# Performance work log

Hardware: AMD Instinct MI355X
Metric: run time of the kernel (lower is better)

Reference implementation:

```python
import jax, jax.numpy as jnp
import numpy as np

L, B, T, C = 4, 4, 2048, 1024
FFN = 4 * C
STD = 0.02
EPS = 1e-5
NEG_INF = -1e38


def setup_inputs() -> dict:
    key = jax.random.key(0)
    ks = jax.random.split(key, 18)
    n = lambda k, shape, s=STD: jax.random.normal(k, shape, jnp.float32) * s
    u = lambda k, shape: jax.random.uniform(k, shape, jnp.float32)
    return {
        "x": jax.random.normal(ks[0], (B, T, C), jnp.float32),
        "ln1_w": jnp.ones((L, C), jnp.float32),
        "tm_mix_k": u(ks[1], (L, 1, 1, C)),
        "tm_mix_v": u(ks[2], (L, 1, 1, C)),
        "tm_mix_r": u(ks[3], (L, 1, 1, C)),
        "tm_k_w": n(ks[4], (L, C, C)),
        "tm_v_w": n(ks[5], (L, C, C)),
        "tm_r_w": n(ks[6], (L, C, C)),
        "tm_o_w": n(ks[7], (L, C, C)),
        # time_decay in [-5, 1] like RWKV decay_speed init; w = -exp(time_decay)
        "time_decay": u(ks[8], (L, C)) * 6.0 - 5.0,
        "time_first": jnp.log(0.3).astype(jnp.float32) + 0.5 * jax.random.normal(ks[9], (L, C), jnp.float32),
        "ln2_w": jnp.ones((L, C), jnp.float32),
        "cm_mix_k": u(ks[10], (L, 1, 1, C)),
        "cm_mix_r": u(ks[11], (L, 1, 1, C)),
        "cm_k_w": n(ks[12], (L, FFN, C)),
        "cm_v_w": n(ks[13], (L, C, FFN)),
        "cm_r_w": n(ks[14], (L, C, C)),
        "lnf_w": jnp.ones((C,), jnp.float32),
    }


def layer_norm(x, w):
    mu = jnp.mean(x, axis=-1, keepdims=True)
    var = jnp.mean(jnp.square(x - mu), axis=-1, keepdims=True)
    return (x - mu) * jax.lax.rsqrt(var + EPS) * w


def time_shift(x):
    # ZeroPad2d((0,0,1,-1)): shift sequence right by one, zero at t=0
    return jnp.pad(x, ((0, 0), (1, 0), (0, 0)))[:, :-1]


def wkv_scan(k, v, time_decay, time_first):
    # k, v: [B, T, C]; numerically-stabilized linear WKV recurrence over T
    w = -jnp.exp(time_decay)  # [C]
    u = time_first            # [C]
    zeros = jnp.zeros(k.shape[::2], k.dtype)  # [B, C]

    def step(carry, kv):
        num, den, mx = carry
        kt, vt = kv
        max_out = jnp.maximum(mx, kt + u)
        e1 = jnp.exp(mx - max_out)
        e2 = jnp.exp(kt + u - max_out)
        out = (e1 * num + e2 * vt) / (e1 * den + e2)
        max_st = jnp.maximum(mx + w, kt)
        e1 = jnp.exp(mx + w - max_st)
        e2 = jnp.exp(kt - max_st)
        return (e1 * num + e2 * vt, e1 * den + e2, max_st), out

    init = (zeros, zeros, jnp.full_like(zeros, NEG_INF))
    _, out = jax.lax.scan(step, init, (k.swapaxes(0, 1), v.swapaxes(0, 1)))
    return out.swapaxes(0, 1)  # [B, T, C]


def reference(x, ln1_w, tm_mix_k, tm_mix_v, tm_mix_r, tm_k_w, tm_v_w, tm_r_w, tm_o_w,
              time_decay, time_first, ln2_w, cm_mix_k, cm_mix_r, cm_k_w, cm_v_w, cm_r_w, lnf_w):
    n_layer = ln1_w.shape[0]
    for l in range(n_layer):
        # --- TimeMixing ---
        h = layer_norm(x, ln1_w[l])
        prev = time_shift(h)
        k = jnp.einsum('btc,oc->bto', h * tm_mix_k[l] + prev * (1 - tm_mix_k[l]), tm_k_w[l])
        v = jnp.einsum('btc,oc->bto', h * tm_mix_v[l] + prev * (1 - tm_mix_v[l]), tm_v_w[l])
        r = jax.nn.sigmoid(jnp.einsum('btc,oc->bto', h * tm_mix_r[l] + prev * (1 - tm_mix_r[l]), tm_r_w[l]))
        wkv = wkv_scan(k, v, time_decay[l], time_first[l])
        x = x + jnp.einsum('btc,oc->bto', r * wkv, tm_o_w[l])
        # --- ChannelMixing ---
        h = layer_norm(x, ln2_w[l])
        prev = time_shift(h)
        kk = jnp.einsum('btc,fc->btf', h * cm_mix_k[l] + prev * (1 - cm_mix_k[l]), cm_k_w[l])  # [B,T,4C]
        vv = jnp.einsum('btf,of->bto', jnp.square(jax.nn.relu(kk)), cm_v_w[l])
        rr = jax.nn.sigmoid(jnp.einsum('btc,oc->bto', h * cm_mix_r[l] + prev * (1 - cm_mix_r[l]), cm_r_w[l]))
        x = x + rr * vv
    return layer_norm(x, lnf_w)
```

## Files before the change

### kernel.cpp

```cpp
#include <hip/hip_runtime.h>
#include <hip/hip_bf16.h>


#define LNUM 4
#define BSZ  4
#define TSZ  2048
#define CSZ  1024
#define FFND 4096
#define MROWS (BSZ*TSZ)
#define EPSF 1e-5f

typedef __hip_bfloat16 bf16;
typedef __bf16 bf16x8 __attribute__((ext_vector_type(8)));
typedef float f32x4 __attribute__((ext_vector_type(4)));

#define BM 128
#define BK 64

#define SCK  64
#define SLEN (TSZ/SCK)

__device__ __forceinline__ void async_copy16(const void* g, void* l) {
    __builtin_amdgcn_global_load_lds((const __attribute__((address_space(1))) void*)g,
                                     (__attribute__((address_space(3))) void*)l, 16, 0, 0);
}

template<int MODE, int TBN>
__launch_bounds__(256)
__global__ void gemm_bt(const bf16* __restrict__ A, const bf16* __restrict__ Bw,
                        void* __restrict__ outp, const bf16* __restrict__ aux,
                        int K, int N)
{
    constexpr int MT  = (TBN == 128) ? 4 : 2;
    constexpr int NBI = TBN / 32;
    __shared__ __align__(16) __bf16 sA[BM*BK];
    __shared__ __align__(16) __bf16 sB[TBN*BK];
    const int tid  = threadIdx.x;
    const int lane = tid & 63;
    const int wid  = tid >> 6;
    const int wmB  = (TBN == 128) ? (wid >> 1) * 64 : wid * 32;
    const int wnB  = (TBN == 128) ? (wid & 1) * 64 : 0;
    const size_t bm0 = (size_t)blockIdx.x * BM;
    const size_t bn0 = (size_t)blockIdx.y * TBN;

    const int lrow8 = lane >> 3;
    const int cbg   = (lane & 7) ^ lrow8;

    const bf16* pA[4]; const bf16* pB[NBI];
#pragma unroll
    for (int i = 0; i < 4; ++i)
        pA[i] = A + (bm0 + (i*4 + wid)*8 + lrow8) * (size_t)K + cbg*8;
#pragma unroll
    for (int i = 0; i < NBI; ++i)
        pB[i] = Bw + (bn0 + (i*4 + wid)*8 + lrow8) * (size_t)K + cbg*8;

    f32x4 acc[MT][4];
#pragma unroll
    for (int a = 0; a < MT; ++a)
#pragma unroll
        for (int b = 0; b < 4; ++b) acc[a][b] = (f32x4){0.f,0.f,0.f,0.f};

    const int q   = lane >> 4;
    const int rlo = lane & 15;

    const int ktiles = K / BK;
    for (int kt = 0; kt < ktiles; ++kt) {
#pragma unroll
        for (int i = 0; i < 4; ++i) {
            async_copy16(pA[i], &sA[(i*4 + wid)*8*BK]);
            pA[i] += BK;
        }
#pragma unroll
        for (int i = 0; i < NBI; ++i) {
            async_copy16(pB[i], &sB[(i*4 + wid)*8*BK]);
            pB[i] += BK;
        }
        __syncthreads();
#pragma unroll
        for (int ks = 0; ks < 2; ++ks) {
            bf16x8 aF[MT], bF[4];
#pragma unroll
            for (int mt = 0; mt < MT; ++mt) {
                const int r  = wmB + mt*16 + rlo;
                const int cb = (ks*4 + q) ^ (r & 7);
                aF[mt] = *(const bf16x8*)&sA[r*BK + cb*8];
            }
#pragma unroll
            for (int nt = 0; nt < 4; ++nt) {
                const int r  = wnB + nt*16 + rlo;
                const int cb = (ks*4 + q) ^ (r & 7);
                bF[nt] = *(const bf16x8*)&sB[r*BK + cb*8];
            }
#pragma unroll
            for (int mt = 0; mt < MT; ++mt)
#pragma unroll
                for (int nt = 0; nt < 4; ++nt)
                    acc[mt][nt] = __builtin_amdgcn_mfma_f32_16x16x32_bf16(
                        aF[mt], bF[nt], acc[mt][nt], 0, 0, 0);
        }
        __syncthreads();
    }

#pragma unroll
    for (int mt = 0; mt < MT; ++mt) {
#pragma unroll
        for (int nt = 0; nt < 4; ++nt) {
            const size_t col = bn0 + wnB + nt*16 + rlo;
#pragma unroll
            for (int i = 0; i < 4; ++i) {
                const size_t row = bm0 + wmB + mt*16 + q*4 + i;
                const size_t idx = row * (size_t)N + col;
                const float v = acc[mt][nt][i];
                if (MODE == 2) {
                    ((float*)outp)[idx] += v;
                } else if (MODE == 3) {
                    const float t = fmaxf(v, 0.f);
                    ((bf16*)outp)[idx] = __float2bfloat16(t*t);
                } else if (MODE == 4) {
                    ((bf16*)outp)[idx] = __float2bfloat16(1.f/(1.f+__expf(-v)));
                } else {
                    ((float*)outp)[idx] += (float)aux[idx] * v;
                }
            }
        }
    }
}

__launch_bounds__(256)
__global__ void gemm_kvr(const bf16* __restrict__ A0, const bf16* __restrict__ A1,
                         const bf16* __restrict__ A2,
                         const bf16* __restrict__ W0, const bf16* __restrict__ W1,
                         const bf16* __restrict__ W2,
                         bf16* __restrict__ O0, bf16* __restrict__ O1,
                         bf16* __restrict__ O2)
{
    constexpr int TBN = 64, MT = 2, NBI = 2, K = CSZ, N = CSZ;
    const int z = blockIdx.z;
    const bf16* A  = (z == 0) ? A0 : (z == 1) ? A1 : A2;
    const bf16* Bw = (z == 0) ? W0 : (z == 1) ? W1 : W2;
    bf16* outp     = (z == 0) ? O0 : (z == 1) ? O1 : O2;

    __shared__ __align__(16) __bf16 sA[BM*BK];
    __shared__ __align__(16) __bf16 sB[TBN*BK];
    const int tid  = threadIdx.x;
    const int lane = tid & 63;
    const int wid  = tid >> 6;
    const int wmB  = wid * 32;
    const size_t bm0 = (size_t)blockIdx.x * BM;
    const size_t bn0 = (size_t)blockIdx.y * TBN;

    const int lrow8 = lane >> 3;
    const int cbg   = (lane & 7) ^ lrow8;

    const bf16* pA[4]; const bf16* pB[NBI];
#pragma unroll
    for (int i = 0; i < 4; ++i)
        pA[i] = A + (bm0 + (i*4 + wid)*8 + lrow8) * (size_t)K + cbg*8;
#pragma unroll
    for (int i = 0; i < NBI; ++i)
        pB[i] = Bw + (bn0 + (i*4 + wid)*8 + lrow8) * (size_t)K + cbg*8;

    f32x4 acc[MT][4];
#pragma unroll
    for (int a = 0; a < MT; ++a)
#pragma unroll
        for (int b = 0; b < 4; ++b) acc[a][b] = (f32x4){0.f,0.f,0.f,0.f};

    const int q   = lane >> 4;
    const int rlo = lane & 15;

    for (int kt = 0; kt < K/BK; ++kt) {
#pragma unroll
        for (int i = 0; i < 4; ++i) {
            async_copy16(pA[i], &sA[(i*4 + wid)*8*BK]);
            pA[i] += BK;
        }
#pragma unroll
        for (int i = 0; i < NBI; ++i) {
            async_copy16(pB[i], &sB[(i*4 + wid)*8*BK]);
            pB[i] += BK;
        }
        __syncthreads();
#pragma unroll
        for (int ks = 0; ks < 2; ++ks) {
            bf16x8 aF[MT], bF[4];
#pragma unroll
            for (int mt = 0; mt < MT; ++mt) {
                const int r  = wmB + mt*16 + rlo;
                const int cb = (ks*4 + q) ^ (r & 7);
                aF[mt] = *(const bf16x8*)&sA[r*BK + cb*8];
            }
#pragma unroll
            for (int nt = 0; nt < 4; ++nt) {
                const int r  = nt*16 + rlo;
                const int cb = (ks*4 + q) ^ (r & 7);
                bF[nt] = *(const bf16x8*)&sB[r*BK + cb*8];
            }
#pragma unroll
            for (int mt = 0; mt < MT; ++mt)
#pragma unroll
                for (int nt = 0; nt < 4; ++nt)
                    acc[mt][nt] = __builtin_amdgcn_mfma_f32_16x16x32_bf16(
                        aF[mt], bF[nt], acc[mt][nt], 0, 0, 0);
        }
        __syncthreads();
    }

#pragma unroll
    for (int mt = 0; mt < MT; ++mt) {
#pragma unroll
        for (int nt = 0; nt < 4; ++nt) {
            const size_t col = bn0 + nt*16 + rlo;
#pragma unroll
            for (int i = 0; i < 4; ++i) {
                const size_t row = bm0 + wmB + mt*16 + q*4 + i;
                float v = acc[mt][nt][i];
                if (z == 2) v = 1.f/(1.f+__expf(-v));
                ((bf16*)outp)[row * (size_t)N + col] = __float2bfloat16(v);
            }
        }
    }
}

template<int NOUT>
__launch_bounds__(256)
__global__ void ln_mix_kernel(const float* __restrict__ x, const float* __restrict__ lnw,
                              const float* __restrict__ mka, const float* __restrict__ mva,
                              const float* __restrict__ mra,
                              bf16* __restrict__ ok, bf16* __restrict__ ov, bf16* __restrict__ orr)
{
    const int bt  = blockIdx.x;
    const int t   = bt % TSZ;
    const int tid = threadIdx.x;
    const float4 xc = ((const float4*)(x + (size_t)bt*CSZ))[tid];
    float4 xp = {0.f,0.f,0.f,0.f};
    const bool hasp = (t != 0);
    if (hasp) xp = ((const float4*)(x + (size_t)(bt-1)*CSZ))[tid];

    float s0 = xc.x+xc.y+xc.z+xc.w;
    float s1 = xc.x*xc.x+xc.y*xc.y+xc.z*xc.z+xc.w*xc.w;
    float s2 = xp.x+xp.y+xp.z+xp.w;
    float s3 = xp.x*xp.x+xp.y*xp.y+xp.z*xp.z+xp.w*xp.w;
#pragma unroll
    for (int off = 32; off > 0; off >>= 1) {
        s0 += __shfl_down(s0, off); s1 += __shfl_down(s1, off);
        s2 += __shfl_down(s2, off); s3 += __shfl_down(s3, off);
    }
    __shared__ float red[4][4];
    if ((tid & 63) == 0) { const int wq = tid >> 6;
        red[wq][0]=s0; red[wq][1]=s1; red[wq][2]=s2; red[wq][3]=s3; }
    __syncthreads();
    s0 = red[0][0]+red[1][0]+red[2][0]+red[3][0];
    s1 = red[0][1]+red[1][1]+red[2][1]+red[3][1];
    s2 = red[0][2]+red[1][2]+red[2][2]+red[3][2];
    s3 = red[0][3]+red[1][3]+red[2][3]+red[3][3];

    const float inv = 1.f/CSZ;
    const float muC = s0*inv;
    const float rsC = rsqrtf(s1*inv - muC*muC + EPSF);
    const float muP = s2*inv;
    const float rsP = rsqrtf(s3*inv - muP*muP + EPSF);

    const int c4 = tid*4;
    const float4 lw = ((const float4*)lnw)[tid];
    const float4 mk = ((const float4*)mka)[tid];
    const float4 mv = (NOUT >= 2) ? ((const float4*)mva)[tid] : lw;
    const float4 mr = (NOUT >= 3) ? ((const float4*)mra)[tid] : lw;

    float hcv[4] = {(xc.x-muC)*rsC*lw.x, (xc.y-muC)*rsC*lw.y,
                    (xc.z-muC)*rsC*lw.z, (xc.w-muC)*rsC*lw.w};
    float hpv[4];
    if (hasp) {
        hpv[0]=(xp.x-muP)*rsP*lw.x; hpv[1]=(xp.y-muP)*rsP*lw.y;
        hpv[2]=(xp.z-muP)*rsP*lw.z; hpv[3]=(xp.w-muP)*rsP*lw.w;
    } else { hpv[0]=hpv[1]=hpv[2]=hpv[3]=0.f; }
    const float mkv[4]={mk.x,mk.y,mk.z,mk.w};
    const float mvv[4]={mv.x,mv.y,mv.z,mv.w};
    const float mrv[4]={mr.x,mr.y,mr.z,mr.w};

    __align__(8) bf16 o0[4], o1[4], o2[4];
#pragma unroll
    for (int j = 0; j < 4; ++j) {
        o0[j] = __float2bfloat16(hcv[j]*mkv[j] + hpv[j]*(1.f-mkv[j]));
        if (NOUT >= 2) o1[j] = __float2bfloat16(hcv[j]*mvv[j] + hpv[j]*(1.f-mvv[j]));
        if (NOUT >= 3) o2[j] = __float2bfloat16(hcv[j]*mrv[j] + hpv[j]*(1.f-mrv[j]));
    }
    *(uint2*)(ok + (size_t)bt*CSZ + c4) = *(const uint2*)o0;
    if (NOUT >= 2) *(uint2*)(ov  + (size_t)bt*CSZ + c4) = *(const uint2*)o1;
    if (NOUT >= 3) *(uint2*)(orr + (size_t)bt*CSZ + c4) = *(const uint2*)o2;
}

__launch_bounds__(256)
__global__ void wkv_sum_kernel(const bf16* __restrict__ kb, const bf16* __restrict__ vb,
                               const float* __restrict__ td,
                               float* __restrict__ sN, float* __restrict__ sD,
                               float* __restrict__ sM)
{
    const int j  = blockIdx.x;
    const int b  = blockIdx.y >> 2;
    const int cg = blockIdx.y & 3;
    const int c  = cg*256 + threadIdx.x;
    const float w = -__expf(td[c]);

    size_t idx = ((size_t)b*TSZ + j*SLEN)*CSZ + c;
    float num = 0.f, den = 0.f, mx = -1e38f;
    float kt = (float)kb[idx], vt = (float)vb[idx];
    for (int t = 0; t < SLEN; ++t) {
        float kn = 0.f, vn = 0.f;
        if (t + 1 < SLEN) {
            kn = (float)kb[idx + CSZ]; vn = (float)vb[idx + CSZ];
        }
        const float ms = fmaxf(mx + w, kt);
        const float p1 = __expf(mx + w - ms);
        const float p2 = __expf(kt - ms);
        num = p1*num + p2*vt; den = p1*den + p2; mx = ms;
        idx += CSZ; kt = kn; vt = vn;
    }
    const size_t sidx = ((size_t)b*SCK + j)*CSZ + c;
    sN[sidx] = num; sD[sidx] = den; sM[sidx] = mx;
}

__launch_bounds__(256)
__global__ void wkv_comb_kernel(const float* __restrict__ td,
                                float* __restrict__ sN, float* __restrict__ sD,
                                float* __restrict__ sM)
{
    const int id = blockIdx.x*256 + threadIdx.x;
    const int b  = id >> 10;
    const int c  = id & (CSZ-1);
    const float wL = -__expf(td[c]) * (float)SLEN;
    float n = 0.f, d = 0.f, m = -1e38f;
    size_t idx = (size_t)b*SCK*CSZ + c;
    float nl = sN[idx], dl = sD[idx], ml = sM[idx];
    for (int j = 0; j < SCK; ++j) {
        float nn = 0.f, dn = 0.f, mn = 0.f;
        if (j + 1 < SCK) {
            nn = sN[idx + CSZ]; dn = sD[idx + CSZ]; mn = sM[idx + CSZ];
        }
        sN[idx] = n; sD[idx] = d; sM[idx] = m;
        const float mi = m + wL;
        const float mo = fmaxf(mi, ml);
        const float e1 = __expf(mi - mo);
        const float e2 = __expf(ml - mo);
        n = e1*n + e2*nl; d = e1*d + e2*dl; m = mo;
        idx += CSZ; nl = nn; dl = dn; ml = mn;
    }
}

__launch_bounds__(256)
__global__ void wkv_out_kernel(const bf16* __restrict__ kb, const bf16* __restrict__ vb,
                               const bf16* __restrict__ rb,
                               const float* __restrict__ td, const float* __restrict__ tf,
                               const float* __restrict__ sN, const float* __restrict__ sD,
                               const float* __restrict__ sM,
                               bf16* __restrict__ outb)
{
    const int j  = blockIdx.x;
    const int b  = blockIdx.y >> 2;
    const int cg = blockIdx.y & 3;
    const int c  = cg*256 + threadIdx.x;
    const float w = -__expf(td[c]);
    const float u = tf[c];

    const size_t sidx = ((size_t)b*SCK + j)*CSZ + c;
    float num = sN[sidx], den = sD[sidx], mx = sM[sidx];

    size_t idx = ((size_t)b*TSZ + j*SLEN)*CSZ + c;
    float kt = (float)kb[idx], vt = (float)vb[idx], rt = (float)rb[idx];
    for (int t = 0; t < SLEN; ++t) {
        float kn = 0.f, vn = 0.f, rn = 0.f;
        if (t + 1 < SLEN) {
            kn = (float)kb[idx + CSZ]; vn = (float)vb[idx + CSZ]; rn = (float)rb[idx + CSZ];
        }
        const float ku = kt + u;
        const float mo = fmaxf(mx, ku);
        const float e1 = __expf(mx - mo);
        const float e2 = __expf(ku - mo);
        const float outv = (e1*num + e2*vt) / (e1*den + e2);
        const float ms = fmaxf(mx + w, kt);
        const float p1 = __expf(mx + w - ms);
        const float p2 = __expf(kt - ms);
        num = p1*num + p2*vt; den = p1*den + p2; mx = ms;
        outb[idx] = __float2bfloat16(rt * outv);
        idx += CSZ; kt = kn; vt = vn; rt = rn;
    }
}

__launch_bounds__(256)
__global__ void final_ln_kernel(const float* __restrict__ x, const float* __restrict__ lnw,
                                float* __restrict__ out)
{
    const int bt  = blockIdx.x;
    const int tid = threadIdx.x;
    const float4 xc = ((const float4*)(x + (size_t)bt*CSZ))[tid];
    float s0 = xc.x+xc.y+xc.z+xc.w;
    float s1 = xc.x*xc.x+xc.y*xc.y+xc.z*xc.z+xc.w*xc.w;
#pragma unroll
    for (int off = 32; off > 0; off >>= 1) {
        s0 += __shfl_down(s0, off); s1 += __shfl_down(s1, off);
    }
    __shared__ float red[4][2];
    if ((tid & 63) == 0) { red[tid>>6][0] = s0; red[tid>>6][1] = s1; }
    __syncthreads();
    s0 = red[0][0]+red[1][0]+red[2][0]+red[3][0];
    s1 = red[0][1]+red[1][1]+red[2][1]+red[3][1];
    const float inv = 1.f/CSZ;
    const float mu = s0*inv;
    const float rs = rsqrtf(s1*inv - mu*mu + EPSF);
    const float4 lw = ((const float4*)lnw)[tid];
    float4 o;
    o.x = (xc.x-mu)*rs*lw.x; o.y = (xc.y-mu)*rs*lw.y;
    o.z = (xc.z-mu)*rs*lw.z; o.w = (xc.w-mu)*rs*lw.w;
    ((float4*)(out + (size_t)bt*CSZ))[tid] = o;
}

#define N4_CC (CSZ*CSZ/4)
#define N4_FC (FFND*CSZ/4)
__global__ void cvt_weights_kernel(const float* __restrict__ tk, const float* __restrict__ tv,
                                   const float* __restrict__ tr, const float* __restrict__ to,
                                   const float* __restrict__ ck, const float* __restrict__ cv,
                                   const float* __restrict__ cr,
                                   bf16* __restrict__ wk, bf16* __restrict__ wv,
                                   bf16* __restrict__ wr, bf16* __restrict__ wo,
                                   bf16* __restrict__ wck, bf16* __restrict__ wcv,
                                   bf16* __restrict__ wcr)
{
    int i = blockIdx.x * 256 + threadIdx.x;
    const float* s; bf16* d;
    if      (i < 1*N4_CC)          { s = tk; d = wk;  }
    else if (i < 2*N4_CC)          { s = tv; d = wv;  i -= 1*N4_CC; }
    else if (i < 3*N4_CC)          { s = tr; d = wr;  i -= 2*N4_CC; }
    else if (i < 4*N4_CC)          { s = to; d = wo;  i -= 3*N4_CC; }
    else if (i < 4*N4_CC+N4_FC)    { s = ck; d = wck; i -= 4*N4_CC; }
    else if (i < 4*N4_CC+2*N4_FC)  { s = cv; d = wcv; i -= 4*N4_CC+N4_FC; }
    else                           { s = cr; d = wcr; i -= 4*N4_CC+2*N4_FC; }
    const float4 f = ((const float4*)s)[i];
    __align__(8) bf16 o[4] = {__float2bfloat16(f.x), __float2bfloat16(f.y),
                              __float2bfloat16(f.z), __float2bfloat16(f.w)};
    ((uint2*)d)[i] = *(const uint2*)o;
}
#define CVT_TOTAL4 (4*N4_CC + 2*N4_FC + N4_CC)

static constexpr size_t SZ_XF32 = (size_t)MROWS*CSZ*4;
static constexpr size_t SZ_ABF  = (size_t)MROWS*CSZ*2;
static constexpr size_t OFF_X   = 0;
static constexpr size_t OFF_XK  = OFF_X  + SZ_XF32;
static constexpr size_t OFF_XV  = OFF_XK + SZ_ABF;
static constexpr size_t OFF_XR  = OFF_XV + SZ_ABF;
static constexpr size_t OFF_K   = OFF_XR + SZ_ABF;
static constexpr size_t OFF_V   = OFF_K  + SZ_ABF;
static constexpr size_t OFF_R   = OFF_V  + SZ_ABF;
static constexpr size_t OFF_KK  = OFF_R  + SZ_ABF;
static constexpr size_t OFF_W   = OFF_KK + (size_t)MROWS*FFND*2;
static constexpr size_t OFF_WK  = OFF_W;
static constexpr size_t OFF_WV  = OFF_WK + (size_t)CSZ*CSZ*2;
static constexpr size_t OFF_WR  = OFF_WV + (size_t)CSZ*CSZ*2;
static constexpr size_t OFF_WO  = OFF_WR + (size_t)CSZ*CSZ*2;
static constexpr size_t OFF_WCK = OFF_WO + (size_t)CSZ*CSZ*2;
static constexpr size_t OFF_WCV = OFF_WCK + (size_t)FFND*CSZ*2;
static constexpr size_t OFF_WCR = OFF_WCV + (size_t)CSZ*FFND*2;

static constexpr size_t SZ_SUM  = (size_t)BSZ*SCK*CSZ*4;

extern "C" void kernel_launch(void* const* d_in, const int* in_sizes, int n_in,
                              void* d_out, int out_size, void* d_ws, size_t ws_size,
                              hipStream_t stream)
{
    const float* xin   = (const float*)d_in[0];
    const float* ln1w  = (const float*)d_in[1];
    const float* tmixk = (const float*)d_in[2];
    const float* tmixv = (const float*)d_in[3];
    const float* tmixr = (const float*)d_in[4];
    const float* tkw   = (const float*)d_in[5];
    const float* tvw   = (const float*)d_in[6];
    const float* trw   = (const float*)d_in[7];
    const float* tow   = (const float*)d_in[8];
    const float* tdec  = (const float*)d_in[9];
    const float* tfst  = (const float*)d_in[10];
    const float* ln2w  = (const float*)d_in[11];
    const float* cmixk = (const float*)d_in[12];
    const float* cmixr = (const float*)d_in[13];
    const float* ckw   = (const float*)d_in[14];
    const float* cvw   = (const float*)d_in[15];
    const float* crw   = (const float*)d_in[16];
    const float* lnfw  = (const float*)d_in[17];

    char* ws = (char*)d_ws;
    float* xres = (float*)(ws + OFF_X);
    bf16* xk  = (bf16*)(ws + OFF_XK);
    bf16* xv  = (bf16*)(ws + OFF_XV);
    bf16* xr  = (bf16*)(ws + OFF_XR);
    bf16* kb  = (bf16*)(ws + OFF_K);
    bf16* vb  = (bf16*)(ws + OFF_V);
    bf16* rb  = (bf16*)(ws + OFF_R);
    bf16* kkb = (bf16*)(ws + OFF_KK);
    bf16* rwkv = xk;
    bf16* rr  = (bf16*)(ws + OFF_K);
    float* sN  = (float*)(ws + OFF_KK);
    float* sD  = (float*)(ws + OFF_KK + SZ_SUM);
    float* sM  = (float*)(ws + OFF_KK + 2*SZ_SUM);
    bf16* wk  = (bf16*)(ws + OFF_WK);
    bf16* wv  = (bf16*)(ws + OFF_WV);
    bf16* wr  = (bf16*)(ws + OFF_WR);
    bf16* wo  = (bf16*)(ws + OFF_WO);
    bf16* wck = (bf16*)(ws + OFF_WCK);
    bf16* wcv = (bf16*)(ws + OFF_WCV);
    bf16* wcr = (bf16*)(ws + OFF_WCR);

    hipMemcpyAsync(xres, xin, SZ_XF32, hipMemcpyDeviceToDevice, stream);

    const dim3 blk(256);
    const dim3 gKVR(MROWS/BM, CSZ/64, 3);
    const dim3 gC64(MROWS/BM, CSZ/64);
    const dim3 gF(MROWS/BM, FFND/128);
    const dim3 gScan(SCK, BSZ*4);

    for (int l = 0; l < LNUM; ++l) {
        const size_t oC  = (size_t)l*CSZ;
        const size_t oCC = (size_t)l*CSZ*CSZ;
        const size_t oFC = (size_t)l*FFND*CSZ;
        cvt_weights_kernel<<<CVT_TOTAL4/256, blk, 0, stream>>>(
            tkw + oCC, tvw + oCC, trw + oCC, tow + oCC,
            ckw + oFC, cvw + oFC, crw + oCC,
            wk, wv, wr, wo, wck, wcv, wcr);

        ln_mix_kernel<3><<<MROWS, blk, 0, stream>>>(xres, ln1w + oC,
            tmixk + oC, tmixv + oC, tmixr + oC, xk, xv, xr);
        gemm_kvr<<<gKVR, blk, 0, stream>>>(xk, xv, xr, wk, wv, wr, kb, vb, rb);
        wkv_sum_kernel<<<gScan, blk, 0, stream>>>(kb, vb, tdec + oC, sN, sD, sM);
        wkv_comb_kernel<<<(BSZ*CSZ)/256, blk, 0, stream>>>(tdec + oC, sN, sD, sM);
        wkv_out_kernel<<<gScan, blk, 0, stream>>>(kb, vb, rb, tdec + oC, tfst + oC,
            sN, sD, sM, rwkv);
        gemm_bt<2,64><<<gC64, blk, 0, stream>>>(rwkv, wo, xres, nullptr, CSZ, CSZ);

        ln_mix_kernel<2><<<MROWS, blk, 0, stream>>>(xres, ln2w + oC,
            cmixk + oC, cmixr + oC, nullptr, xk, xv, nullptr);
        gemm_bt<3,128><<<gF, blk, 0, stream>>>(xk, wck, kkb, nullptr, CSZ, FFND);
        gemm_bt<4,64><<<gC64, blk, 0, stream>>>(xv, wcr, rr, nullptr, CSZ, CSZ);
        gemm_bt<5,64><<<gC64, blk, 0, stream>>>(kkb, wcv, xres, rr, FFND, CSZ);
    }
    final_ln_kernel<<<MROWS, blk, 0, stream>>>(xres, lnfw, (float*)d_out);
}
```

Measured before the change: 1.673 ms.

## Double-buffer LDS tiles in GEMM kernels to overlap global loads with MFMA

Both GEMM kernels now keep two LDS buffers per operand and prefetch the next K tile with async global-to-LDS copies while the current tile is consumed by MFMA. Partial vmcnt waits leave the newest tile's loads in flight, and raw s_barrier calls replace __syncthreads. This hides global load latency behind compute. In exchange it doubles LDS use per block, which may lower occupancy, and it relies on hand-counted waitcnt values being correct.

```diff
diff --git a/kernel.cpp b/kernel.cpp
--- a/kernel.cpp
+++ b/kernel.cpp
@@ -20,6 +20,8 @@
 #define SCK  64
 #define SLEN (TSZ/SCK)
 
+#define WAITCNT_VM(N) asm volatile("s_waitcnt vmcnt(" #N ")" ::: "memory")
+
 __device__ __forceinline__ void async_copy16(const void* g, void* l) {
     __builtin_amdgcn_global_load_lds((const __attribute__((address_space(1))) void*)g,
                                      (__attribute__((address_space(3))) void*)l, 16, 0, 0);
@@ -33,8 +35,9 @@
 {
     constexpr int MT  = (TBN == 128) ? 4 : 2;
     constexpr int NBI = TBN / 32;
-    __shared__ __align__(16) __bf16 sA[BM*BK];
-    __shared__ __align__(16) __bf16 sB[TBN*BK];
+    constexpr int NI  = 4 + NBI;
+    __shared__ __align__(16) __bf16 sA[2*BM*BK];
+    __shared__ __align__(16) __bf16 sB[2*TBN*BK];
     const int tid  = threadIdx.x;
     const int lane = tid & 63;
     const int wid  = tid >> 6;
@@ -64,18 +67,40 @@
     const int rlo = lane & 15;
 
     const int ktiles = K / BK;
+
+#pragma unroll
+    for (int i = 0; i < 4; ++i) {
+        async_copy16(pA[i], &sA[(i*4 + wid)*8*BK]);
+        pA[i] += BK;
+    }
+#pragma unroll
+    for (int i = 0; i < NBI; ++i) {
+        async_copy16(pB[i], &sB[(i*4 + wid)*8*BK]);
+        pB[i] += BK;
+    }
+
     for (int kt = 0; kt < ktiles; ++kt) {
-#pragma unroll
-        for (int i = 0; i < 4; ++i) {
-            async_copy16(pA[i], &sA[(i*4 + wid)*8*BK]);
-            pA[i] += BK;
-        }
-#pragma unroll
-        for (int i = 0; i < NBI; ++i) {
-            async_copy16(pB[i], &sB[(i*4 + wid)*8*BK]);
-            pB[i] += BK;
-        }
-        __syncthreads();
+        const int cur = kt & 1;
+        const int nxt = cur ^ 1;
+        if (kt + 1 < ktiles) {
+#pragma unroll
+            for (int i = 0; i < 4; ++i) {
+                async_copy16(pA[i], &sA[nxt*(BM*BK) + (i*4 + wid)*8*BK]);
+                pA[i] += BK;
+            }
+#pragma unroll
+            for (int i = 0; i < NBI; ++i) {
+                async_copy16(pB[i], &sB[nxt*(TBN*BK) + (i*4 + wid)*8*BK]);
+                pB[i] += BK;
+            }
+            if constexpr (NI == 8) WAITCNT_VM(8); else WAITCNT_VM(6);
+        } else {
+            WAITCNT_VM(0);
+        }
+        __builtin_amdgcn_s_barrier();
+
+        const __bf16* bAp = sA + cur*(BM*BK);
+        const __bf16* bBp = sB + cur*(TBN*BK);
 #pragma unroll
         for (int ks = 0; ks < 2; ++ks) {
             bf16x8 aF[MT], bF[4];
@@ -83,13 +108,13 @@
             for (int mt = 0; mt < MT; ++mt) {
                 const int r  = wmB + mt*16 + rlo;
                 const int cb = (ks*4 + q) ^ (r & 7);
-                aF[mt] = *(const bf16x8*)&sA[r*BK + cb*8];
+                aF[mt] = *(const bf16x8*)&bAp[r*BK + cb*8];
             }
 #pragma unroll
             for (int nt = 0; nt < 4; ++nt) {
                 const int r  = wnB + nt*16 + rlo;
                 const int cb = (ks*4 + q) ^ (r & 7);
-                bF[nt] = *(const bf16x8*)&sB[r*BK + cb*8];
+                bF[nt] = *(const bf16x8*)&bBp[r*BK + cb*8];
             }
 #pragma unroll
             for (int mt = 0; mt < MT; ++mt)
@@ -98,7 +123,8 @@
                     acc[mt][nt] = __builtin_amdgcn_mfma_f32_16x16x32_bf16(
                         aF[mt], bF[nt], acc[mt][nt], 0, 0, 0);
         }
-        __syncthreads();
+        asm volatile("" ::: "memory");
+        __builtin_amdgcn_s_barrier();
     }
 
 #pragma unroll
@@ -140,8 +166,8 @@
     const bf16* Bw = (z == 0) ? W0 : (z == 1) ? W1 : W2;
     bf16* outp     = (z == 0) ? O0 : (z == 1) ? O1 : O2;
 
-    __shared__ __align__(16) __bf16 sA[BM*BK];
-    __shared__ __align__(16) __bf16 sB[TBN*BK];
+    __shared__ __align__(16) __bf16 sA[2*BM*BK];
+    __shared__ __align__(16) __bf16 sB[2*TBN*BK];
     const int tid  = threadIdx.x;
     const int lane = tid & 63;
     const int wid  = tid >> 6;
@@ -169,18 +195,41 @@
     const int q   = lane >> 4;
     const int rlo = lane & 15;
 
-    for (int kt = 0; kt < K/BK; ++kt) {
-#pragma unroll
-        for (int i = 0; i < 4; ++i) {
-            async_copy16(pA[i], &sA[(i*4 + wid)*8*BK]);
-            pA[i] += BK;
-        }
-#pragma unroll
-        for (int i = 0; i < NBI; ++i) {
-            async_copy16(pB[i], &sB[(i*4 + wid)*8*BK]);
-            pB[i] += BK;
-        }
-        __syncthreads();
+    constexpr int ktiles = K / BK;
+
+#pragma unroll
+    for (int i = 0; i < 4; ++i) {
+        async_copy16(pA[i], &sA[(i*4 + wid)*8*BK]);
+        pA[i] += BK;
+    }
+#pragma unroll
+    for (int i = 0; i < NBI; ++i) {
+        async_copy16(pB[i], &sB[(i*4 + wid)*8*BK]);
+        pB[i] += BK;
+    }
+
+    for (int kt = 0; kt < ktiles; ++kt) {
+        const int cur = kt & 1;
+        const int nxt = cur ^ 1;
+        if (kt + 1 < ktiles) {
+#pragma unroll
+            for (int i = 0; i < 4; ++i) {
+                async_copy16(pA[i], &sA[nxt*(BM*BK) + (i*4 + wid)*8*BK]);
+                pA[i] += BK;
+            }
+#pragma unroll
+            for (int i = 0; i < NBI; ++i) {
+                async_copy16(pB[i], &sB[nxt*(TBN*BK) + (i*4 + wid)*8*BK]);
+                pB[i] += BK;
+            }
+            WAITCNT_VM(6);
+        } else {
+            WAITCNT_VM(0);
+        }
+        __builtin_amdgcn_s_barrier();
+
+        const __bf16* bAp = sA + cur*(BM*BK);
+        const __bf16* bBp = sB + cur*(TBN*BK);
 #pragma unroll
         for (int ks = 0; ks < 2; ++ks) {
             bf16x8 aF[MT], bF[4];
@@ -188,13 +237,13 @@
             for (int mt = 0; mt < MT; ++mt) {
                 const int r  = wmB + mt*16 + rlo;
                 const int cb = (ks*4 + q) ^ (r & 7);
-                aF[mt] = *(const bf16x8*)&sA[r*BK + cb*8];
+                aF[mt] = *(const bf16x8*)&bAp[r*BK + cb*8];
             }
 #pragma unroll
             for (int nt = 0; nt < 4; ++nt) {
                 const int r  = nt*16 + rlo;
                 const int cb = (ks*4 + q) ^ (r & 7);
-                bF[nt] = *(const bf16x8*)&sB[r*BK + cb*8];
+                bF[nt] = *(const bf16x8*)&bBp[r*BK + cb*8];
             }
 #pragma unroll
             for (int mt = 0; mt < MT; ++mt)
@@ -203,7 +252,8 @@
                     acc[mt][nt] = __builtin_amdgcn_mfma_f32_16x16x32_bf16(
                         aF[mt], bF[nt], acc[mt][nt], 0, 0, 0);
         }
-        __syncthreads();
+        asm volatile("" ::: "memory");
+        __builtin_amdgcn_s_barrier();
     }
 
 #pragma unroll
```

Result: slower. 1.882 ms (+12.5%).
